# Performance work log

Measured on AMD Instinct MI355X. Metric: run time of the kernel, lower is better.

Reference implementation:

```python
import jax, jax.numpy as jnp
import numpy as np

N_NODES = 100000
N_EDGES = 6400000
NUM_FEATURES = 50
HID1, HID2 = 30, 25


def setup_inputs() -> dict:
    key = jax.random.key(0)
    k_x, k_e, k_w1, k_b1, k_w2, k_b2 = jax.random.split(key, 6)
    x = jax.random.normal(k_x, (N_NODES, NUM_FEATURES), dtype=jnp.float32)
    edge_index = jax.random.randint(k_e, (2, N_EDGES), 0, N_NODES, dtype=jnp.int64)
    # Glorot-style init like PyG GCNConv
    W1 = jax.random.normal(k_w1, (NUM_FEATURES, HID1), dtype=jnp.float32) * (1.0 / np.sqrt(NUM_FEATURES))
    b1 = jnp.zeros((HID1,), dtype=jnp.float32)
    W2 = jax.random.normal(k_w2, (HID1, HID2), dtype=jnp.float32) * (1.0 / np.sqrt(HID1))
    b2 = jnp.zeros((HID2,), dtype=jnp.float32)
    return {"x": x, "edge_index": edge_index, "W1": W1, "b1": b1, "W2": W2, "b2": b2}


def reference(x, edge_index, W1, b1, W2, b2):
    """Two-layer GCN (PyG GCNConv semantics, eval mode so dropout is identity).

    GCNConv: out = D^{-1/2} (A + I) D^{-1/2} (x @ W) + b,
    with messages flowing source (row) -> target (col).
    """
    N = x.shape[0]
    loop = jnp.arange(N, dtype=edge_index.dtype)
    src = jnp.concatenate([edge_index[0], loop])  # [E+N]
    dst = jnp.concatenate([edge_index[1], loop])  # [E+N]
    # degree (incl. self-loops) at target nodes; >= 1 so rsqrt is safe
    deg = jax.ops.segment_sum(jnp.ones_like(dst, dtype=x.dtype), dst, num_segments=N)
    dinv = jax.lax.rsqrt(deg)
    norm = dinv[src] * dinv[dst]  # [E+N]

    def gcn_layer(h, W, b):
        h = h @ W                                   # [N, F_out] small GEMM
        msgs = norm[:, None] * h[src]               # gather + scale
        agg = jax.ops.segment_sum(msgs, dst, num_segments=N)  # scatter-add
        return agg + b

    h = jax.nn.relu(gcn_layer(x, W1, b1))
    # F.dropout with training=False is identity (eval-mode reference)
    return gcn_layer(h, W2, b2)
```

## Files before the change

### kernel.cpp

```cpp
#include <hip/hip_runtime.h>
#include <hip/hip_bf16.h>
#include <hip/hip_fp16.h>

#define NN 100000
#define NE 6400000
#define F_IN 50
#define H1 30
#define H2 25

#define BSZ 128
#define NB 782
#define NBLK 256
#define CHUNK 25000
#define EPT ((CHUNK + 1023) / 1024)
#define EPTB 12
#define CAP (EPTB * 1024)
#define CAPB 9216

__global__ __launch_bounds__(1024) void k_init(int* __restrict__ gcur) {
    int i = threadIdx.x;
    if (i < NB) gcur[i] = i * CAPB;
}

__global__ __launch_bounds__(1024) void k_place2(const int* __restrict__ src,
                                                 const int* __restrict__ dst,
                                                 int* __restrict__ gcur,
                                                 int* __restrict__ ebuf) {
    __shared__ int keys[CHUNK];
    __shared__ int cnt[NB];
    __shared__ int lstart[NB];
    __shared__ int gbase[NB];
    __shared__ int scanT[1024];
    int t = threadIdx.x;
    int base = blockIdx.x * CHUNK;
    for (int i = t; i < NB; i += 1024) cnt[i] = 0;
    __syncthreads();
    int sreg[EPT], breg[EPT];
#pragma unroll
    for (int k = 0; k < EPT; ++k) {
        int idx = k * 1024 + t;
        if (idx < CHUNK) {
            int d = dst[base + idx];
            int s = src[base + idx];
            breg[k] = d >> 7;
            sreg[k] = (s << 7) | (d & 127);
            atomicAdd(&cnt[breg[k]], 1);
        }
    }
    __syncthreads();
    int v = (t < NB) ? cnt[t] : 0;
    scanT[t] = v;
    __syncthreads();
    for (int off = 1; off < 1024; off <<= 1) {
        int u = (t >= off) ? scanT[t - off] : 0;
        __syncthreads();
        scanT[t] += u;
        __syncthreads();
    }
    if (t < NB) {
        int e = scanT[t] - v;
        lstart[t] = e;
        cnt[t] = e;
        gbase[t] = atomicAdd(&gcur[t], v);
    }
    __syncthreads();
#pragma unroll
    for (int k = 0; k < EPT; ++k) {
        int idx = k * 1024 + t;
        if (idx < CHUNK) {
            int p = atomicAdd(&cnt[breg[k]], 1);
            keys[p] = sreg[k];
        }
    }
    __syncthreads();
    int wv = t >> 6, ln = t & 63;
    for (int b = wv; b < NB; b += 16) {
        int s0 = lstart[b], e0 = cnt[b], gb = gbase[b];
        int lim = (b + 1) * CAPB;
        int cnt_run = e0 - s0;
        if (gb + cnt_run > lim) cnt_run = lim - gb;
        for (int off = ln; off < cnt_run; off += 64)
            ebuf[gb + off] = keys[s0 + off];
    }
}

__global__ __launch_bounds__(1024) void k_bsort(int* __restrict__ ebuf,
                                                const int* __restrict__ gcur,
                                                int* __restrict__ rowptr,
                                                int* __restrict__ rowend) {
    __shared__ int cnt[BSZ];
    __shared__ int loc[BSZ];
    int b = blockIdx.x;
    int beg = b * CAPB;
    int end = gcur[b];
    int m = end - beg; if (m > CAP) m = CAP;
    int t = threadIdx.x;
    if (t < BSZ) cnt[t] = 0;
    __syncthreads();
    int keys[EPTB];
#pragma unroll
    for (int k = 0; k < EPTB; ++k) {
        int idx = k * 1024 + t;
        if (idx < m) {
            int key = ebuf[beg + idx];
            keys[k] = key;
            atomicAdd(&cnt[key & 127], 1);
        }
    }
    __syncthreads();
    if (t < BSZ) loc[t] = cnt[t];
    __syncthreads();
    for (int off = 1; off < BSZ; off <<= 1) {
        int v = (t < BSZ && t >= off) ? loc[t - off] : 0;
        __syncthreads();
        if (t < BSZ) loc[t] += v;
        __syncthreads();
    }
    int nbase = b * BSZ;
    int nloc = NN - nbase; if (nloc > BSZ) nloc = BSZ;
    if (t < nloc) {
        rowptr[nbase + t] = beg + loc[t] - cnt[t];
        rowend[nbase + t] = beg + loc[t];
    }
    __syncthreads();
    if (t < BSZ) cnt[t] = beg + loc[t] - cnt[t];
    __syncthreads();
#pragma unroll
    for (int k = 0; k < EPTB; ++k) {
        int idx = k * 1024 + t;
        if (idx < m) {
            int key = keys[k];
            int p = atomicAdd(&cnt[key & 127], 1);
            ebuf[p] = key >> 7;
        }
    }
}

__global__ __launch_bounds__(256) void k_gemm1(const float* __restrict__ x,
                                               const float* __restrict__ W1,
                                               const int* __restrict__ rowptr,
                                               const int* __restrict__ rowend,
                                               __half* __restrict__ h1lo,
                                               __half* __restrict__ h1hi) {
    __shared__ float Wp[F_IN * 32];
    __shared__ float xs[16 * F_IN];
    __shared__ float dns[16];
    int t = threadIdx.x;
    for (int i = t; i < F_IN * 32; i += 256) {
        int k = i >> 5, j = i & 31;
        Wp[i] = (j < H1) ? W1[k * H1 + j] : 0.f;
    }
    int nbase = blockIdx.x * 16;
    for (int i = t; i < 16 * F_IN; i += 256)
        xs[i] = x[nbase * F_IN + i];
    if (t < 16) {
        int n = nbase + t;
        dns[t] = rsqrtf((float)(rowend[n] - rowptr[n] + 1));
    }
    __syncthreads();
    int g = t >> 4;
    int l = t & 15;
    float a0 = 0.f, a1 = 0.f;
#pragma unroll
    for (int k = 0; k < F_IN; ++k) {
        float xk = xs[g * F_IN + k];
        float2 w = *(const float2*)&Wp[k * 32 + 2 * l];
        a0 = fmaf(xk, w.x, a0);
        a1 = fmaf(xk, w.y, a1);
    }
    float dn = dns[g];
    __half2 hh = __halves2half2(__float2half(dn * a0), __float2half(dn * a1));
    int n = nbase + g;
    if (l < 8) *(__half2*)&h1lo[n * 16 + 2 * l] = hh;
    else       *(__half2*)&h1hi[n * 16 + 2 * (l - 8)] = hh;
}

__global__ __launch_bounds__(256) void k_aggh1(const int* __restrict__ ebuf,
                                               const int* __restrict__ rowptr,
                                               const int* __restrict__ rowend,
                                               const __half* __restrict__ tab,
                                               const float* __restrict__ b1,
                                               int fbase,
                                               __half* __restrict__ a_buf) {
    __shared__ float bb[16];
    if (threadIdx.x < 16) {
        int j = fbase + threadIdx.x;
        bb[threadIdx.x] = (j < H1) ? b1[j] : 0.f;
    }
    __syncthreads();
    int g = threadIdx.x >> 3;
    int l = threadIdx.x & 7;
    int n = blockIdx.x * 32 + g;
    int beg = rowptr[n], end = rowend[n];
    int m = end - beg;
    int nfull = m & ~7;
    float ax = 0.f, ay = 0.f;
    for (int base = beg; base < beg + nfull; base += 8) {
        int sv = ebuf[base + l];
        int ss[8]; __half2 vv[8];
#pragma unroll
        for (int u = 0; u < 8; ++u) ss[u] = __shfl(sv, u, 8);
#pragma unroll
        for (int u = 0; u < 8; ++u) vv[u] = *(const __half2*)&tab[ss[u] * 16 + 2 * l];
#pragma unroll
        for (int u = 0; u < 8; ++u) { float2 f = __half22float2(vv[u]); ax += f.x; ay += f.y; }
    }
    int rem = m - nfull;
    if (rem) {
        int sv = (l < rem) ? ebuf[beg + nfull + l] : 0;
        for (int i = 0; i < rem; ++i) {
            int s = __shfl(sv, i, 8);
            float2 f = __half22float2(*(const __half2*)&tab[s * 16 + 2 * l]);
            ax += f.x; ay += f.y;
        }
    }
    float dn = rsqrtf((float)(m + 1));
    float2 self = __half22float2(*(const __half2*)&tab[n * 16 + 2 * l]);
    int j0 = fbase + 2 * l, j1 = j0 + 1;
    float v0 = (j0 < H1) ? fmaxf(dn * (ax + self.x) + bb[2 * l], 0.f) : 0.f;
    float v1 = (j1 < H1) ? fmaxf(dn * (ay + self.y) + bb[2 * l + 1], 0.f) : 0.f;
    *(__half2*)&a_buf[n * 32 + fbase + 2 * l] =
        __halves2half2(__float2half(v0), __float2half(v1));
}

__global__ __launch_bounds__(256) void k_gemm2(const __half* __restrict__ a_buf,
                                               const float* __restrict__ W2,
                                               const int* __restrict__ rowptr,
                                               const int* __restrict__ rowend,
                                               __half* __restrict__ t2lo,
                                               __half* __restrict__ t2hi) {
    __shared__ float Wp[H1 * 32];
    __shared__ float as2[16 * 33];
    __shared__ float dns[16];
    int t = threadIdx.x;
    for (int i = t; i < H1 * 32; i += 256) {
        int k = i >> 5, j = i & 31;
        Wp[i] = (j < H2) ? W2[k * H2 + j] : 0.f;
    }
    int nbase = blockIdx.x * 16;
    {
        __half2 hv = *(const __half2*)&a_buf[nbase * 32 + 2 * t];
        float2 f = __half22float2(hv);
        int r = t >> 4;
        int c = (t & 15) * 2;
        as2[r * 33 + c]     = f.x;
        as2[r * 33 + c + 1] = f.y;
    }
    if (t < 16) {
        int n = nbase + t;
        dns[t] = rsqrtf((float)(rowend[n] - rowptr[n] + 1));
    }
    __syncthreads();
    int g = t >> 4;
    int l = t & 15;
    float a0 = 0.f, a1 = 0.f;
#pragma unroll
    for (int k = 0; k < H1; ++k) {
        float ak = as2[g * 33 + k];
        float2 w = *(const float2*)&Wp[k * 32 + 2 * l];
        a0 = fmaf(ak, w.x, a0);
        a1 = fmaf(ak, w.y, a1);
    }
    float dn = dns[g];
    __half2 hh = __halves2half2(__float2half(dn * a0), __float2half(dn * a1));
    int n = nbase + g;
    if (l < 8) *(__half2*)&t2lo[n * 16 + 2 * l] = hh;
    else       *(__half2*)&t2hi[n * 16 + 2 * (l - 8)] = hh;
}

__global__ __launch_bounds__(256) void k_aggh2(const int* __restrict__ ebuf,
                                               const int* __restrict__ rowptr,
                                               const int* __restrict__ rowend,
                                               const __half* __restrict__ tab,
                                               const float* __restrict__ b2,
                                               int fbase,
                                               float* __restrict__ out) {
    __shared__ float bb[16];
    if (threadIdx.x < 16) {
        int j = fbase + threadIdx.x;
        bb[threadIdx.x] = (j < H2) ? b2[j] : 0.f;
    }
    __syncthreads();
    int g = threadIdx.x >> 3;
    int l = threadIdx.x & 7;
    int n = blockIdx.x * 32 + g;
    int beg = rowptr[n], end = rowend[n];
    int m = end - beg;
    int nfull = m & ~7;
    float ax = 0.f, ay = 0.f;
    for (int base = beg; base < beg + nfull; base += 8) {
        int sv = ebuf[base + l];
        int ss[8]; __half2 vv[8];
#pragma unroll
        for (int u = 0; u < 8; ++u) ss[u] = __shfl(sv, u, 8);
#pragma unroll
        for (int u = 0; u < 8; ++u) vv[u] = *(const __half2*)&tab[ss[u] * 16 + 2 * l];
#pragma unroll
        for (int u = 0; u < 8; ++u) { float2 f = __half22float2(vv[u]); ax += f.x; ay += f.y; }
    }
    int rem = m - nfull;
    if (rem) {
        int sv = (l < rem) ? ebuf[beg + nfull + l] : 0;
        for (int i = 0; i < rem; ++i) {
            int s = __shfl(sv, i, 8);
            float2 f = __half22float2(*(const __half2*)&tab[s * 16 + 2 * l]);
            ax += f.x; ay += f.y;
        }
    }
    float dn = rsqrtf((float)(m + 1));
    float2 self = __half22float2(*(const __half2*)&tab[n * 16 + 2 * l]);
    int j0 = fbase + 2 * l, j1 = j0 + 1;
    if (j0 < H2) out[n * H2 + j0] = dn * (ax + self.x) + bb[2 * l];
    if (j1 < H2) out[n * H2 + j1] = dn * (ay + self.y) + bb[2 * l + 1];
}

extern "C" void kernel_launch(void* const* d_in, const int* in_sizes, int n_in,
                              void* d_out, int out_size, void* d_ws, size_t ws_size,
                              hipStream_t stream) {
    const float* x   = (const float*)d_in[0];
    const int*   ei  = (const int*)d_in[1];
    const float* W1  = (const float*)d_in[2];
    const float* b1  = (const float*)d_in[3];
    const float* W2  = (const float*)d_in[4];
    const float* b2  = (const float*)d_in[5];
    float*       out = (float*)d_out;

    const int* src = ei;
    const int* dst = ei + NE;

    char* ws = (char*)d_ws;
    int*    rowptr = (int*)   (ws + 0);
    int*    rowend = (int*)   (ws + 400128);
    int*    gcur   = (int*)   (ws + 800256);
    __half* h1lo   = (__half*)(ws + 803456);
    __half* h1hi   = (__half*)(ws + 4003456);
    __half* abuf   = (__half*)(ws + 7203456);
    __half* t2lo   = (__half*)(ws + 13603456);
    __half* t2hi   = (__half*)(ws + 16803456);
    int*    ebuf   = (int*)   (ws + 20003456);

    k_init  <<<1, 1024, 0, stream>>>(gcur);
    k_place2<<<NBLK, 1024, 0, stream>>>(src, dst, gcur, ebuf);
    k_bsort <<<NB, 1024, 0, stream>>>(ebuf, gcur, rowptr, rowend);
    k_gemm1 <<<NN / 16, 256, 0, stream>>>(x, W1, rowptr, rowend, h1lo, h1hi);
    k_aggh1 <<<NN / 32, 256, 0, stream>>>(ebuf, rowptr, rowend, h1lo, b1, 0,  abuf);
    k_aggh1 <<<NN / 32, 256, 0, stream>>>(ebuf, rowptr, rowend, h1hi, b1, 16, abuf);
    k_gemm2 <<<NN / 16, 256, 0, stream>>>(abuf, W2, rowptr, rowend, t2lo, t2hi);
    k_aggh2 <<<NN / 32, 256, 0, stream>>>(ebuf, rowptr, rowend, t2lo, b2, 0,  out);
    k_aggh2 <<<NN / 32, 256, 0, stream>>>(ebuf, rowptr, rowend, t2hi, b2, 16, out);
}
```

Measured before the change: 287.2 us.

## Merge split half-feature tables into one 32-wide table and single aggregation pass

Drops the lo/hi 16-feature split of the per-node fp16 tables and stores one 64-byte row per node. Each layer now runs one aggregation kernel instead of two, with each lane gathering 4 halves (8 bytes) per edge rather than 2. This halves the passes over the edge list and the launches, at the cost of a per-node gather footprint twice as large. The original split was probably there to keep each table L2-resident, so the merged table may lose some cache locality.

```diff
diff --git a/kernel.cpp b/kernel.cpp
--- a/kernel.cpp
+++ b/kernel.cpp
@@ -16,6 +16,16 @@
 #define EPTB 12
 #define CAP (EPTB * 1024)
 #define CAPB 9216
+
+__device__ __forceinline__ float2 h2f2(unsigned int u) {
+    __half2 h;
+    *reinterpret_cast<unsigned int*>(&h) = u;
+    return __half22float2(h);
+}
+__device__ __forceinline__ unsigned int f2h2(float a, float b) {
+    __half2 h = __halves2half2(__float2half(a), __float2half(b));
+    return *reinterpret_cast<unsigned int*>(&h);
+}
 
 __global__ __launch_bounds__(1024) void k_init(int* __restrict__ gcur) {
     int i = threadIdx.x;
@@ -140,8 +150,7 @@
                                                const float* __restrict__ W1,
                                                const int* __restrict__ rowptr,
                                                const int* __restrict__ rowend,
-                                               __half* __restrict__ h1lo,
-                                               __half* __restrict__ h1hi) {
+                                               __half* __restrict__ h1p) {
     __shared__ float Wp[F_IN * 32];
     __shared__ float xs[16 * F_IN];
     __shared__ float dns[16];
@@ -169,24 +178,19 @@
         a1 = fmaf(xk, w.y, a1);
     }
     float dn = dns[g];
-    __half2 hh = __halves2half2(__float2half(dn * a0), __float2half(dn * a1));
     int n = nbase + g;
-    if (l < 8) *(__half2*)&h1lo[n * 16 + 2 * l] = hh;
-    else       *(__half2*)&h1hi[n * 16 + 2 * (l - 8)] = hh;
-}
-
-__global__ __launch_bounds__(256) void k_aggh1(const int* __restrict__ ebuf,
-                                               const int* __restrict__ rowptr,
-                                               const int* __restrict__ rowend,
-                                               const __half* __restrict__ tab,
-                                               const float* __restrict__ b1,
-                                               int fbase,
-                                               __half* __restrict__ a_buf) {
-    __shared__ float bb[16];
-    if (threadIdx.x < 16) {
-        int j = fbase + threadIdx.x;
-        bb[threadIdx.x] = (j < H1) ? b1[j] : 0.f;
-    }
+    *(__half2*)&h1p[n * 32 + 2 * l] =
+        __halves2half2(__float2half(dn * a0), __float2half(dn * a1));
+}
+
+__global__ __launch_bounds__(256) void k_agg1(const int* __restrict__ ebuf,
+                                              const int* __restrict__ rowptr,
+                                              const int* __restrict__ rowend,
+                                              const __half* __restrict__ tab,
+                                              const float* __restrict__ b1,
+                                              __half* __restrict__ a_buf) {
+    __shared__ float bb[32];
+    if (threadIdx.x < 32) bb[threadIdx.x] = (threadIdx.x < H1) ? b1[threadIdx.x] : 0.f;
     __syncthreads();
     int g = threadIdx.x >> 3;
     int l = threadIdx.x & 7;
@@ -194,41 +198,47 @@
     int beg = rowptr[n], end = rowend[n];
     int m = end - beg;
     int nfull = m & ~7;
-    float ax = 0.f, ay = 0.f;
+    float a0 = 0.f, a1 = 0.f, a2 = 0.f, a3 = 0.f;
     for (int base = beg; base < beg + nfull; base += 8) {
         int sv = ebuf[base + l];
-        int ss[8]; __half2 vv[8];
+        int ss[8]; uint2 vv[8];
 #pragma unroll
         for (int u = 0; u < 8; ++u) ss[u] = __shfl(sv, u, 8);
 #pragma unroll
-        for (int u = 0; u < 8; ++u) vv[u] = *(const __half2*)&tab[ss[u] * 16 + 2 * l];
-#pragma unroll
-        for (int u = 0; u < 8; ++u) { float2 f = __half22float2(vv[u]); ax += f.x; ay += f.y; }
+        for (int u = 0; u < 8; ++u) vv[u] = *(const uint2*)&tab[ss[u] * 32 + 4 * l];
+#pragma unroll
+        for (int u = 0; u < 8; ++u) {
+            float2 f0 = h2f2(vv[u].x), f1 = h2f2(vv[u].y);
+            a0 += f0.x; a1 += f0.y; a2 += f1.x; a3 += f1.y;
+        }
     }
     int rem = m - nfull;
     if (rem) {
         int sv = (l < rem) ? ebuf[beg + nfull + l] : 0;
         for (int i = 0; i < rem; ++i) {
             int s = __shfl(sv, i, 8);
-            float2 f = __half22float2(*(const __half2*)&tab[s * 16 + 2 * l]);
-            ax += f.x; ay += f.y;
+            uint2 v = *(const uint2*)&tab[s * 32 + 4 * l];
+            float2 f0 = h2f2(v.x), f1 = h2f2(v.y);
+            a0 += f0.x; a1 += f0.y; a2 += f1.x; a3 += f1.y;
         }
     }
     float dn = rsqrtf((float)(m + 1));
-    float2 self = __half22float2(*(const __half2*)&tab[n * 16 + 2 * l]);
-    int j0 = fbase + 2 * l, j1 = j0 + 1;
-    float v0 = (j0 < H1) ? fmaxf(dn * (ax + self.x) + bb[2 * l], 0.f) : 0.f;
-    float v1 = (j1 < H1) ? fmaxf(dn * (ay + self.y) + bb[2 * l + 1], 0.f) : 0.f;
-    *(__half2*)&a_buf[n * 32 + fbase + 2 * l] =
-        __halves2half2(__float2half(v0), __float2half(v1));
+    uint2 sf = *(const uint2*)&tab[n * 32 + 4 * l];
+    float2 s0 = h2f2(sf.x), s1 = h2f2(sf.y);
+    int j = 4 * l;
+    float v0 = fmaxf(dn * (a0 + s0.x) + bb[j],     0.f);
+    float v1 = fmaxf(dn * (a1 + s0.y) + bb[j + 1], 0.f);
+    float v2 = fmaxf(dn * (a2 + s1.x) + bb[j + 2], 0.f);
+    float v3 = fmaxf(dn * (a3 + s1.y) + bb[j + 3], 0.f);
+    uint2 o; o.x = f2h2(v0, v1); o.y = f2h2(v2, v3);
+    *(uint2*)&a_buf[n * 32 + j] = o;
 }
 
 __global__ __launch_bounds__(256) void k_gemm2(const __half* __restrict__ a_buf,
                                                const float* __restrict__ W2,
                                                const int* __restrict__ rowptr,
                                                const int* __restrict__ rowend,
-                                               __half* __restrict__ t2lo,
-                                               __half* __restrict__ t2hi) {
+                                               __half* __restrict__ t2p) {
     __shared__ float Wp[H1 * 32];
     __shared__ float as2[16 * 33];
     __shared__ float dns[16];
@@ -262,24 +272,19 @@
         a1 = fmaf(ak, w.y, a1);
     }
     float dn = dns[g];
-    __half2 hh = __halves2half2(__float2half(dn * a0), __float2half(dn * a1));
     int n = nbase + g;
-    if (l < 8) *(__half2*)&t2lo[n * 16 + 2 * l] = hh;
-    else       *(__half2*)&t2hi[n * 16 + 2 * (l - 8)] = hh;
-}
-
-__global__ __launch_bounds__(256) void k_aggh2(const int* __restrict__ ebuf,
-                                               const int* __restrict__ rowptr,
-                                               const int* __restrict__ rowend,
-                                               const __half* __restrict__ tab,
-                                               const float* __restrict__ b2,
-                                               int fbase,
-                                               float* __restrict__ out) {
-    __shared__ float bb[16];
-    if (threadIdx.x < 16) {
-        int j = fbase + threadIdx.x;
-        bb[threadIdx.x] = (j < H2) ? b2[j] : 0.f;
-    }
+    *(__half2*)&t2p[n * 32 + 2 * l] =
+        __halves2half2(__float2half(dn * a0), __float2half(dn * a1));
+}
+
+__global__ __launch_bounds__(256) void k_agg2(const int* __restrict__ ebuf,
+                                              const int* __restrict__ rowptr,
+                                              const int* __restrict__ rowend,
+                                              const __half* __restrict__ tab,
+                                              const float* __restrict__ b2,
+                                              float* __restrict__ out) {
+    __shared__ float bb[32];
+    if (threadIdx.x < 32) bb[threadIdx.x] = (threadIdx.x < H2) ? b2[threadIdx.x] : 0.f;
     __syncthreads();
     int g = threadIdx.x >> 3;
     int l = threadIdx.x & 7;
@@ -287,31 +292,38 @@
     int beg = rowptr[n], end = rowend[n];
     int m = end - beg;
     int nfull = m & ~7;
-    float ax = 0.f, ay = 0.f;
+    float a0 = 0.f, a1 = 0.f, a2 = 0.f, a3 = 0.f;
     for (int base = beg; base < beg + nfull; base += 8) {
         int sv = ebuf[base + l];
-        int ss[8]; __half2 vv[8];
+        int ss[8]; uint2 vv[8];
 #pragma unroll
         for (int u = 0; u < 8; ++u) ss[u] = __shfl(sv, u, 8);
 #pragma unroll
-        for (int u = 0; u < 8; ++u) vv[u] = *(const __half2*)&tab[ss[u] * 16 + 2 * l];
-#pragma unroll
-        for (int u = 0; u < 8; ++u) { float2 f = __half22float2(vv[u]); ax += f.x; ay += f.y; }
+        for (int u = 0; u < 8; ++u) vv[u] = *(const uint2*)&tab[ss[u] * 32 + 4 * l];
+#pragma unroll
+        for (int u = 0; u < 8; ++u) {
+            float2 f0 = h2f2(vv[u].x), f1 = h2f2(vv[u].y);
+            a0 += f0.x; a1 += f0.y; a2 += f1.x; a3 += f1.y;
+        }
     }
     int rem = m - nfull;
     if (rem) {
         int sv = (l < rem) ? ebuf[beg + nfull + l] : 0;
         for (int i = 0; i < rem; ++i) {
             int s = __shfl(sv, i, 8);
-            float2 f = __half22float2(*(const __half2*)&tab[s * 16 + 2 * l]);
-            ax += f.x; ay += f.y;
+            uint2 v = *(const uint2*)&tab[s * 32 + 4 * l];
+            float2 f0 = h2f2(v.x), f1 = h2f2(v.y);
+            a0 += f0.x; a1 += f0.y; a2 += f1.x; a3 += f1.y;
         }
     }
     float dn = rsqrtf((float)(m + 1));
-    float2 self = __half22float2(*(const __half2*)&tab[n * 16 + 2 * l]);
-    int j0 = fbase + 2 * l, j1 = j0 + 1;
-    if (j0 < H2) out[n * H2 + j0] = dn * (ax + self.x) + bb[2 * l];
-    if (j1 < H2) out[n * H2 + j1] = dn * (ay + self.y) + bb[2 * l + 1];
+    uint2 sf = *(const uint2*)&tab[n * 32 + 4 * l];
+    float2 s0 = h2f2(sf.x), s1 = h2f2(sf.y);
+    int j = 4 * l;
+    if (j < H2)     out[n * H2 + j]     = dn * (a0 + s0.x) + bb[j];
+    if (j + 1 < H2) out[n * H2 + j + 1] = dn * (a1 + s0.y) + bb[j + 1];
+    if (j + 2 < H2) out[n * H2 + j + 2] = dn * (a2 + s1.x) + bb[j + 2];
+    if (j + 3 < H2) out[n * H2 + j + 3] = dn * (a3 + s1.y) + bb[j + 3];
 }
 
 extern "C" void kernel_launch(void* const* d_in, const int* in_sizes, int n_in,
@@ -332,20 +344,16 @@
     int*    rowptr = (int*)   (ws + 0);
     int*    rowend = (int*)   (ws + 400128);
     int*    gcur   = (int*)   (ws + 800256);
-    __half* h1lo   = (__half*)(ws + 803456);
-    __half* h1hi   = (__half*)(ws + 4003456);
+    __half* h1p    = (__half*)(ws + 803456);
     __half* abuf   = (__half*)(ws + 7203456);
-    __half* t2lo   = (__half*)(ws + 13603456);
-    __half* t2hi   = (__half*)(ws + 16803456);
+    __half* t2p    = (__half*)(ws + 13603456);
     int*    ebuf   = (int*)   (ws + 20003456);
 
     k_init  <<<1, 1024, 0, stream>>>(gcur);
     k_place2<<<NBLK, 1024, 0, stream>>>(src, dst, gcur, ebuf);
     k_bsort <<<NB, 1024, 0, stream>>>(ebuf, gcur, rowptr, rowend);
-    k_gemm1 <<<NN / 16, 256, 0, stream>>>(x, W1, rowptr, rowend, h1lo, h1hi);
-    k_aggh1 <<<NN / 32, 256, 0, stream>>>(ebuf, rowptr, rowend, h1lo, b1, 0,  abuf);
-    k_aggh1 <<<NN / 32, 256, 0, stream>>>(ebuf, rowptr, rowend, h1hi, b1, 16, abuf);
-    k_gemm2 <<<NN / 16, 256, 0, stream>>>(abuf, W2, rowptr, rowend, t2lo, t2hi);
-    k_aggh2 <<<NN / 32, 256, 0, stream>>>(ebuf, rowptr, rowend, t2lo, b2, 0,  out);
-    k_aggh2 <<<NN / 32, 256, 0, stream>>>(ebuf, rowptr, rowend, t2hi, b2, 16, out);
-}
+    k_gemm1 <<<NN / 16, 256, 0, stream>>>(x, W1, rowptr, rowend, h1p);
+    k_agg1  <<<NN / 32, 256, 0, stream>>>(ebuf, rowptr, rowend, h1p, b1, abuf);
+    k_gemm2 <<<NN / 16, 256, 0, stream>>>(abuf, W2, rowptr, rowend, t2p);
+    k_agg2  <<<NN / 32, 256, 0, stream>>>(ebuf, rowptr, rowend, t2p, b2, out);
+}
```

Measured after the change: 252.5 us, median of 2. 1.14x faster.
